# Kernel optimization log

Hardware: AMD Instinct MI355X
Metric: run time of the kernel (lower is better)

## Reference

```python
import jax, jax.numpy as jnp
import numpy as np

V, C, BLK = 32000, 512, 2048
B, T = 4, 2048
EPS = 1e-5


def _layernorm(x, g, b):
    mu = jnp.mean(x, axis=-1, keepdims=True)
    var = jnp.mean(jnp.square(x - mu), axis=-1, keepdims=True)
    return (x - mu) * jax.lax.rsqrt(var + EPS) * g + b


def setup_inputs() -> dict:
    key = jax.random.key(0)
    ks = jax.random.split(key, 16)
    s = 0.02
    return {
        "idx": jax.random.randint(ks[0], (B, T), 0, V),
        "targets": jax.random.randint(ks[1], (B, T), 0, V),
        "tok_emb": jax.random.normal(ks[2], (V, C), jnp.float32) * s,
        "pos_emb": jax.random.normal(ks[3], (BLK, C), jnp.float32) * s,
        "Wk": jax.random.normal(ks[4], (C, C), jnp.float32) * s,
        "Wq": jax.random.normal(ks[5], (C, C), jnp.float32) * s,
        "Wv": jax.random.normal(ks[6], (C, C), jnp.float32) * s,
        "W1": jax.random.normal(ks[7], (4 * C, C), jnp.float32) * s,
        "b1": jnp.zeros((4 * C,), jnp.float32),
        "W2": jax.random.normal(ks[8], (C, 4 * C), jnp.float32) * s,
        "b2": jnp.zeros((C,), jnp.float32),
        "g1": jnp.ones((C,), jnp.float32),
        "beta1": jnp.zeros((C,), jnp.float32),
        "g2": jnp.ones((C,), jnp.float32),
        "beta2": jnp.zeros((C,), jnp.float32),
        "Wlm": jax.random.normal(ks[9], (V, C), jnp.float32) * s,
        "blm": jnp.zeros((V,), jnp.float32),
    }


def reference(idx, targets, tok_emb, pos_emb, Wk, Wq, Wv, W1, b1, W2, b2,
              g1, beta1, g2, beta2, Wlm, blm):
    # embeddings
    x = tok_emb[idx] + pos_emb[:T]  # [B,T,C]
    # single-head causal self-attention (dropout = identity, eval mode)
    h = _layernorm(x, g1, beta1)
    q = jnp.einsum('btc,dc->btd', h, Wq)
    k = jnp.einsum('btc,dc->btd', h, Wk)
    v = jnp.einsum('btc,dc->btd', h, Wv)
    wei = jnp.einsum('btd,bsd->bts', q, k) * (C ** -0.5)  # [B,T,T]
    mask = jnp.tril(jnp.ones((T, T), bool))
    wei = jnp.where(mask, wei, -jnp.inf)
    wei = jax.nn.softmax(wei, axis=-1)
    x = x + jnp.einsum('bts,bsd->btd', wei, v)
    # FFN
    h2 = _layernorm(x, g2, beta2)
    ff = jax.nn.relu(jnp.einsum('btc,fc->btf', h2, W1) + b1)
    x = x + jnp.einsum('btf,cf->btc', ff, W2) + b2
    # lm head + cross-entropy
    logits = (jnp.einsum('btc,vc->btv', x, Wlm) + blm).reshape(B * T, V)
    logp = jax.nn.log_softmax(logits, axis=-1)
    loss = -jnp.mean(jnp.take_along_axis(logp, targets.reshape(-1, 1), axis=1))
    return logits, loss
```

## Files before the change

kernel.cpp:

```cpp
#include <hip/hip_runtime.h>

typedef __bf16 bf16;
typedef __bf16 bf16x8 __attribute__((ext_vector_type(8)));
typedef float  f32x4  __attribute__((ext_vector_type(4)));

#define NB 4
#define NT 2048
#define NC 512
#define NV 32000
#define NROWS (NB*NT)
#define NCHUNK (NV/128)
#define LNEPS 1e-5f

static __device__ __forceinline__ void load_lds16(const bf16* g, bf16* l) {
  __builtin_amdgcn_global_load_lds(
      (const __attribute__((address_space(1))) void*)g,
      (__attribute__((address_space(3))) void*)l, 16, 0, 0);
}

__global__ __launch_bounds__(256)
void cvt_kernel(const float* __restrict__ in, bf16* __restrict__ out, int n8) {
  long i = (long)blockIdx.x * 256 + threadIdx.x;
  long stride = (long)gridDim.x * 256;
  for (; i < n8; i += stride) {
    const float* p = in + i * 8;
    f32x4 a = *(const f32x4*)p;
    f32x4 b = *(const f32x4*)(p + 4);
    bf16x8 o;
    o[0]=(bf16)a.x; o[1]=(bf16)a.y; o[2]=(bf16)a.z; o[3]=(bf16)a.w;
    o[4]=(bf16)b.x; o[5]=(bf16)b.y; o[6]=(bf16)b.z; o[7]=(bf16)b.w;
    *(bf16x8*)(out + i*8) = o;
  }
}

__global__ __launch_bounds__(64)
void embed_kernel(const int* __restrict__ idx, const float* __restrict__ tok,
                  const float* __restrict__ pos, float* __restrict__ x0) {
  int row = blockIdx.x;
  int t = row & (NT-1);
  int id = idx[row];
  int lane = threadIdx.x;
  const float* tr = tok + (long)id*NC + lane*8;
  const float* pr = pos + (long)t*NC + lane*8;
  f32x4 a0 = *(const f32x4*)tr, a1 = *(const f32x4*)(tr+4);
  f32x4 p0 = *(const f32x4*)pr, p1 = *(const f32x4*)(pr+4);
  f32x4 r0 = a0 + p0, r1 = a1 + p1;
  float* o = x0 + (long)row*NC + lane*8;
  *(f32x4*)o = r0; *(f32x4*)(o+4) = r1;
}

__global__ __launch_bounds__(64)
void ln_kernel(const float* __restrict__ x, const float* __restrict__ gw,
               const float* __restrict__ bw, bf16* __restrict__ out) {
  int row = blockIdx.x;
  int lane = threadIdx.x;
  const float* xr = x + (long)row*NC + lane*8;
  f32x4 a = *(const f32x4*)xr;
  f32x4 b = *(const f32x4*)(xr+4);
  float v[8] = {a.x,a.y,a.z,a.w,b.x,b.y,b.z,b.w};
  float s = 0.f;
  #pragma unroll
  for (int j=0;j<8;++j) s += v[j];
  #pragma unroll
  for (int m=32;m>=1;m>>=1) s += __shfl_xor(s, m);
  float mu = s * (1.f/NC);
  float sq = 0.f;
  #pragma unroll
  for (int j=0;j<8;++j) { v[j] -= mu; sq += v[j]*v[j]; }
  #pragma unroll
  for (int m=32;m>=1;m>>=1) sq += __shfl_xor(sq, m);
  float rs = rsqrtf(sq * (1.f/NC) + LNEPS);
  const float* gp = gw + lane*8;
  const float* bp = bw + lane*8;
  f32x4 g0 = *(const f32x4*)gp, g1 = *(const f32x4*)(gp+4);
  f32x4 b0 = *(const f32x4*)bp, b1 = *(const f32x4*)(bp+4);
  float gg[8] = {g0.x,g0.y,g0.z,g0.w,g1.x,g1.y,g1.z,g1.w};
  float bb[8] = {b0.x,b0.y,b0.z,b0.w,b1.x,b1.y,b1.z,b1.w};
  bf16x8 o;
  #pragma unroll
  for (int j=0;j<8;++j) o[j] = (bf16)(v[j]*rs*gg[j] + bb[j]);
  *(bf16x8*)(out + (long)row*NC + lane*8) = o;
}

__global__ __launch_bounds__(256)
void transpose_kernel(const bf16* __restrict__ v, bf16* __restrict__ vt) {
  __shared__ bf16 tile[64][66];
  int b = blockIdx.z;
  int t0 = blockIdx.x*64, c0 = blockIdx.y*64;
  int tid = threadIdx.x;
  int r = tid >> 2, ch = (tid & 3) * 16;
  const bf16* src = v + ((long)b*NT + t0 + r)*NC + c0 + ch;
  #pragma unroll
  for (int i=0;i<16;++i) tile[r][ch+i] = src[i];
  __syncthreads();
  bf16x8 o0, o1;
  #pragma unroll
  for (int i=0;i<8;++i) o0[i] = tile[ch+i][r];
  #pragma unroll
  for (int i=0;i<8;++i) o1[i] = tile[ch+8+i][r];
  bf16* dst = vt + ((long)b*NC + c0 + r)*NT + t0 + ch;
  *(bf16x8*)dst = o0;
  *(bf16x8*)(dst+8) = o1;
}

__global__ __launch_bounds__(256)
void softmax_kernel(float* __restrict__ S) {
  const int row = blockIdx.x;
  const int t = row & (NT-1);
  const int tid = threadIdx.x;
  float* sr = S + (long)row*NT;
  bf16* pr = (bf16*)S + (long)row*(2*NT);
  const float scale = 0.044194173824159216f;
  f32x4 v0 = *(const f32x4*)(sr + tid*8);
  f32x4 v1 = *(const f32x4*)(sr + tid*8 + 4);
  float v[8] = {v0.x,v0.y,v0.z,v0.w,v1.x,v1.y,v1.z,v1.w};
  int cb = tid*8;
  float mx = -1e30f;
  #pragma unroll
  for (int j=0;j<8;++j) {
    v[j] = (cb + j <= t) ? v[j]*scale : -1e30f;
    mx = fmaxf(mx, v[j]);
  }
  __shared__ float redm[4];
  #pragma unroll
  for (int m=32;m>=1;m>>=1) mx = fmaxf(mx, __shfl_xor(mx, m));
  if ((tid & 63) == 0) redm[tid>>6] = mx;
  __syncthreads();
  mx = fmaxf(fmaxf(redm[0],redm[1]), fmaxf(redm[2],redm[3]));
  float e[8]; float s = 0.f;
  #pragma unroll
  for (int j=0;j<8;++j) { e[j] = (cb + j <= t) ? __expf(v[j]-mx) : 0.f; s += e[j]; }
  __shared__ float reds[4];
  #pragma unroll
  for (int m=32;m>=1;m>>=1) s += __shfl_xor(s, m);
  if ((tid & 63) == 0) reds[tid>>6] = s;
  __syncthreads();
  s = reds[0]+reds[1]+reds[2]+reds[3];
  float inv = 1.f/s;
  bf16x8 o;
  #pragma unroll
  for (int j=0;j<8;++j) o[j] = (bf16)(e[j]*inv);
  *(bf16x8*)(pr + cb) = o;
}

enum { EPI_F32=0, EPI_BF16=1, EPI_BIAS_RELU_BF16=2, EPI_BIAS_RES_BF16=3, EPI_RES_F32=4, EPI_LMHEAD=5 };

template<int EPI>
__global__ __launch_bounds__(256)
void gemm_bt(const bf16* __restrict__ A, const bf16* __restrict__ B, int K,
             long lda, long ldb, long sAb, long sBb,
             float* __restrict__ outf, bf16* __restrict__ outb, long ldo, long sOb,
             const float* __restrict__ bias,
             const float* __restrict__ res, long ldr, long sRb,
             float* __restrict__ pmax, float* __restrict__ psum, int nchunk) {
  __shared__ bf16 As[128*32] __attribute__((aligned(16)));
  __shared__ bf16 Bs[128*32] __attribute__((aligned(16)));
  const int tid = threadIdx.x;
  const int wave = tid >> 6;
  const int lane = tid & 63;
  const int bm = blockIdx.y, bn = blockIdx.x, bz = blockIdx.z;
  const int wr = wave >> 1, wc = wave & 1;
  const int l15 = lane & 15, g = lane >> 4;

  const bf16* Ab = A + (long)bz*sAb + (long)bm*128*lda;
  const bf16* Bb = B + (long)bz*sBb + (long)bn*128*ldb;

  f32x4 acc[4][4] = {};

  const int r0 = tid >> 2,          c0 = tid & 3;
  const int r1 = (256+tid) >> 2,    c1 = tid & 3;
  bf16* lA0 = As + (wave*64)*8;
  bf16* lB0 = Bs + (wave*64)*8;
  bf16* lA1 = As + (256 + wave*64)*8;
  bf16* lB1 = Bs + (256 + wave*64)*8;

  for (int k0 = 0; k0 < K; k0 += 32) {
    __syncthreads();
    load_lds16(Ab + (long)r0*lda + k0 + c0*8, lA0);
    load_lds16(Bb + (long)r0*ldb + k0 + c0*8, lB0);
    load_lds16(Ab + (long)r1*lda + k0 + c1*8, lA1);
    load_lds16(Bb + (long)r1*ldb + k0 + c1*8, lB1);
    __syncthreads();
    bf16x8 af[4], bfr[4];
    #pragma unroll
    for (int m=0;m<4;++m)
      af[m] = *(const bf16x8*)(As + ((wr*64 + m*16 + l15)*32 + g*8));
    #pragma unroll
    for (int n=0;n<4;++n)
      bfr[n] = *(const bf16x8*)(Bs + ((wc*64 + n*16 + l15)*32 + g*8));
    #pragma unroll
    for (int m=0;m<4;++m)
      #pragma unroll
      for (int n=0;n<4;++n)
        acc[m][n] = __builtin_amdgcn_mfma_f32_16x16x32_bf16(af[m], bfr[n], acc[m][n], 0, 0, 0);
  }

  const long rowbase = (long)bm*128 + wr*64;
  const long colbase = (long)bn*128 + wc*64;

  if constexpr (EPI == EPI_LMHEAD) {
    __shared__ float redm[2][128];
    __shared__ float reds[2][128];
    #pragma unroll
    for (int m=0;m<4;++m) {
      #pragma unroll
      for (int n=0;n<4;++n) {
        long c = colbase + n*16 + l15;
        float bv = bias[c];
        #pragma unroll
        for (int reg=0;reg<4;++reg) {
          acc[m][n][reg] += bv;
          long rr = rowbase + m*16 + g*4 + reg;
          outf[rr*ldo + c] = acc[m][n][reg];
        }
      }
    }
    #pragma unroll
    for (int m=0;m<4;++m) {
      #pragma unroll
      for (int reg=0;reg<4;++reg) {
        float mx = -1e30f;
        #pragma unroll
        for (int n=0;n<4;++n) mx = fmaxf(mx, acc[m][n][reg]);
        #pragma unroll
        for (int msk=8;msk>=1;msk>>=1) mx = fmaxf(mx, __shfl_xor(mx, msk));
        float se = 0.f;
        #pragma unroll
        for (int n=0;n<4;++n) se += __expf(acc[m][n][reg] - mx);
        #pragma unroll
        for (int msk=8;msk>=1;msk>>=1) se += __shfl_xor(se, msk);
        if (l15 == 0) {
          int lr = wr*64 + m*16 + g*4 + reg;
          redm[wc][lr] = mx;
          reds[wc][lr] = se;
        }
      }
    }
    __syncthreads();
    if (tid < 128) {
      float m0 = redm[0][tid], m1 = redm[1][tid];
      float M = fmaxf(m0, m1);
      float Sv = reds[0][tid]*__expf(m0 - M) + reds[1][tid]*__expf(m1 - M);
      long row = (long)bm*128 + tid;
      pmax[row*nchunk + bn] = M;
      psum[row*nchunk + bn] = Sv;
    }
  } else {
    #pragma unroll
    for (int m=0;m<4;++m) {
      #pragma unroll
      for (int n=0;n<4;++n) {
        long c = colbase + n*16 + l15;
        #pragma unroll
        for (int reg=0;reg<4;++reg) {
          long rr = rowbase + m*16 + g*4 + reg;
          float v = acc[m][n][reg];
          if constexpr (EPI == EPI_F32) {
            outf[(long)bz*sOb + rr*ldo + c] = v;
          } else if constexpr (EPI == EPI_BF16) {
            outb[(long)bz*sOb + rr*ldo + c] = (bf16)v;
          } else if constexpr (EPI == EPI_BIAS_RELU_BF16) {
            v += bias[c];
            v = fmaxf(v, 0.f);
            outb[rr*ldo + c] = (bf16)v;
          } else if constexpr (EPI == EPI_BIAS_RES_BF16) {
            v += bias[c] + res[rr*ldr + c];
            outb[rr*ldo + c] = (bf16)v;
          } else if constexpr (EPI == EPI_RES_F32) {
            v += res[(long)bz*sRb + rr*ldr + c];
            outf[(long)bz*sOb + rr*ldo + c] = v;
          }
        }
      }
    }
  }
}

__global__ __launch_bounds__(256)
void loss1_kernel(const float* __restrict__ pmax, const float* __restrict__ psum,
                  const float* __restrict__ logits, const int* __restrict__ targets,
                  float* __restrict__ rowloss) {
  int row = blockIdx.x;
  int tid = threadIdx.x;
  int lane = tid & 63, wv = tid >> 6;
  float cm = (tid < NCHUNK) ? pmax[(long)row*NCHUNK + tid] : -1e30f;
  float cs = (tid < NCHUNK) ? psum[(long)row*NCHUNK + tid] : 0.f;
  float mx = cm;
  #pragma unroll
  for (int m=32;m>=1;m>>=1) mx = fmaxf(mx, __shfl_xor(mx, m));
  __shared__ float rm[4];
  if (lane == 0) rm[wv] = mx;
  __syncthreads();
  float M = fmaxf(fmaxf(rm[0],rm[1]), fmaxf(rm[2],rm[3]));
  float sc = cs * __expf(cm - M);
  #pragma unroll
  for (int m=32;m>=1;m>>=1) sc += __shfl_xor(sc, m);
  __shared__ float rs_[4];
  if (lane == 0) rs_[wv] = sc;
  __syncthreads();
  if (tid == 0) {
    float Sv = rs_[0]+rs_[1]+rs_[2]+rs_[3];
    float lse = M + logf(Sv);
    int tgt = targets[row];
    float lg = logits[(long)row*NV + tgt];
    rowloss[row] = lse - lg;
  }
}

__global__ __launch_bounds__(256)
void loss2_kernel(const float* __restrict__ rowloss, float* __restrict__ out) {
  int tid = threadIdx.x;
  float s = 0.f;
  for (int i = tid; i < NROWS; i += 256) s += rowloss[i];
  #pragma unroll
  for (int m=32;m>=1;m>>=1) s += __shfl_xor(s, m);
  __shared__ float rs_[4];
  if ((tid & 63) == 0) rs_[tid>>6] = s;
  __syncthreads();
  if (tid == 0) out[0] = (rs_[0]+rs_[1]+rs_[2]+rs_[3]) * (1.f/NROWS);
}

extern "C" void kernel_launch(void* const* d_in, const int* in_sizes, int n_in,
                              void* d_out, int out_size, void* d_ws, size_t ws_size,
                              hipStream_t stream) {
  const int*   idx  = (const int*)d_in[0];
  const int*   tgt  = (const int*)d_in[1];
  const float* tok  = (const float*)d_in[2];
  const float* pos  = (const float*)d_in[3];
  const float* Wk   = (const float*)d_in[4];
  const float* Wq   = (const float*)d_in[5];
  const float* Wv   = (const float*)d_in[6];
  const float* W1   = (const float*)d_in[7];
  const float* b1   = (const float*)d_in[8];
  const float* W2   = (const float*)d_in[9];
  const float* b2   = (const float*)d_in[10];
  const float* g1   = (const float*)d_in[11];
  const float* be1  = (const float*)d_in[12];
  const float* g2   = (const float*)d_in[13];
  const float* be2  = (const float*)d_in[14];
  const float* Wlm  = (const float*)d_in[15];
  const float* blm  = (const float*)d_in[16];

  float* logits = (float*)d_out;
  float* loss   = logits + (long)NROWS*NV;

  char* w = (char*)d_ws;
  auto alloc = [&](size_t bytes) -> char* {
    char* p = w; w += (bytes + 255) & ~(size_t)255; return p;
  };
  bf16* wqb  = (bf16*)alloc((size_t)NC*NC*2);
  bf16* wkb  = (bf16*)alloc((size_t)NC*NC*2);
  bf16* wvb  = (bf16*)alloc((size_t)NC*NC*2);
  bf16* w1b  = (bf16*)alloc((size_t)4*NC*NC*2);
  bf16* w2b  = (bf16*)alloc((size_t)4*NC*NC*2);
  bf16* wlmb = (bf16*)alloc((size_t)NV*NC*2);
  float* x0  = (float*)alloc((size_t)NROWS*NC*4);
  bf16* h1b  = (bf16*)alloc((size_t)NROWS*NC*2);
  bf16* qb   = (bf16*)alloc((size_t)NROWS*NC*2);
  bf16* kb   = (bf16*)alloc((size_t)NROWS*NC*2);
  bf16* vb   = (bf16*)alloc((size_t)NROWS*NC*2);
  bf16* vtb  = (bf16*)alloc((size_t)NROWS*NC*2);
  float* Sb  = (float*)alloc((size_t)NB*NT*NT*4);
  float* x1  = (float*)alloc((size_t)NROWS*NC*4);
  bf16* h2b  = (bf16*)alloc((size_t)NROWS*NC*2);
  bf16* ffb  = (bf16*)alloc((size_t)NROWS*4*NC*2);
  bf16* x2b  = (bf16*)alloc((size_t)NROWS*NC*2);
  float* pmax = (float*)alloc((size_t)NROWS*NCHUNK*4);
  float* psum = (float*)alloc((size_t)NROWS*NCHUNK*4);
  float* rowloss = (float*)alloc((size_t)NROWS*4);

  auto cvt = [&](const float* in, bf16* out, long n) {
    int n8 = (int)(n/8);
    int blocks = (n8 + 255)/256; if (blocks > 2048) blocks = 2048;
    cvt_kernel<<<blocks, 256, 0, stream>>>(in, out, n8);
  };
  cvt(Wq, wqb, (long)NC*NC);
  cvt(Wk, wkb, (long)NC*NC);
  cvt(Wv, wvb, (long)NC*NC);
  cvt(W1, w1b, (long)4*NC*NC);
  cvt(W2, w2b, (long)4*NC*NC);
  cvt(Wlm, wlmb, (long)NV*NC);

  embed_kernel<<<NROWS, 64, 0, stream>>>(idx, tok, pos, x0);
  ln_kernel<<<NROWS, 64, 0, stream>>>(x0, g1, be1, h1b);

  gemm_bt<EPI_BF16><<<dim3(4,64,1), 256, 0, stream>>>(
      h1b, wqb, NC, NC, NC, 0, 0, nullptr, qb, NC, 0,
      nullptr, nullptr, 0, 0, nullptr, nullptr, 0);
  gemm_bt<EPI_BF16><<<dim3(4,64,1), 256, 0, stream>>>(
      h1b, wkb, NC, NC, NC, 0, 0, nullptr, kb, NC, 0,
      nullptr, nullptr, 0, 0, nullptr, nullptr, 0);
  gemm_bt<EPI_BF16><<<dim3(4,64,1), 256, 0, stream>>>(
      h1b, wvb, NC, NC, NC, 0, 0, nullptr, vb, NC, 0,
      nullptr, nullptr, 0, 0, nullptr, nullptr, 0);

  transpose_kernel<<<dim3(NT/64, NC/64, NB), 256, 0, stream>>>(vb, vtb);

  gemm_bt<EPI_F32><<<dim3(16,16,NB), 256, 0, stream>>>(
      qb, kb, NC, NC, NC, (long)NT*NC, (long)NT*NC,
      Sb, nullptr, NT, (long)NT*NT,
      nullptr, nullptr, 0, 0, nullptr, nullptr, 0);

  softmax_kernel<<<NROWS, 256, 0, stream>>>(Sb);

  gemm_bt<EPI_RES_F32><<<dim3(4,16,NB), 256, 0, stream>>>(
      (const bf16*)Sb, vtb, NT, 2*NT, NT, (long)NT*2*NT, (long)NC*NT,
      x1, nullptr, NC, (long)NT*NC,
      nullptr, x0, NC, (long)NT*NC, nullptr, nullptr, 0);

  ln_kernel<<<NROWS, 64, 0, stream>>>(x1, g2, be2, h2b);

  gemm_bt<EPI_BIAS_RELU_BF16><<<dim3(16,64,1), 256, 0, stream>>>(
      h2b, w1b, NC, NC, NC, 0, 0, nullptr, ffb, 4*NC, 0,
      b1, nullptr, 0, 0, nullptr, nullptr, 0);

  gemm_bt<EPI_BIAS_RES_BF16><<<dim3(4,64,1), 256, 0, stream>>>(
      ffb, w2b, 4*NC, 4*NC, 4*NC, 0, 0, nullptr, x2b, NC, 0,
      b2, x1, NC, 0, nullptr, nullptr, 0);

  gemm_bt<EPI_LMHEAD><<<dim3(NCHUNK,64,1), 256, 0, stream>>>(
      x2b, wlmb, NC, NC, NC, 0, 0, logits, nullptr, NV, 0,
      blm, nullptr, 0, 0, pmax, psum, NCHUNK);

  loss1_kernel<<<NROWS, 256, 0, stream>>>(pmax, psum, logits, tgt, rowloss);
  loss2_kernel<<<1, 256, 0, stream>>>(rowloss, loss);
}
```

Baseline: 887.9 us.

## Replace GEMM with 256x256 double-buffered swizzled kernel, fuse QKV, skip causal tiles

Replaces the 128x128 single-buffered GEMM with a 256x256-tile, 512-thread kernel. It uses 128KB of double-buffered LDS with XOR swizzle, interleaved barriers and setprio to overlap global->LDS loads with MFMA. The Q/K/V projections are fused into one GEMM with a concatenated weight. The causal QK^T skips upper-triangle tiles and the PV GEMM limits K to the causal extent. The LM head uses XCD-aware block remapping. Risks include lower occupancy, added register pressure from 32 accumulators per thread, and nkt_eff needing to be even for the two-tile loop.

```diff
diff --git a/kernel.cpp b/kernel.cpp
--- a/kernel.cpp
+++ b/kernel.cpp
@@ -9,13 +9,20 @@
 #define NC 512
 #define NV 32000
 #define NROWS (NB*NT)
-#define NCHUNK (NV/128)
+#define NCHUNK (NV/256)
 #define LNEPS 1e-5f
-
-static __device__ __forceinline__ void load_lds16(const bf16* g, bf16* l) {
+#define SMEM_B 131072
+
+static __device__ __forceinline__ void load_lds16(const bf16* g, char* l) {
   __builtin_amdgcn_global_load_lds(
       (const __attribute__((address_space(1))) void*)g,
       (__attribute__((address_space(3))) void*)l, 16, 0, 0);
+}
+
+static __device__ __forceinline__ void bar() {
+  asm volatile("" ::: "memory");
+  __builtin_amdgcn_s_barrier();
+  asm volatile("" ::: "memory");
 }
 
 __global__ __launch_bounds__(256)
@@ -83,13 +90,13 @@
 }
 
 __global__ __launch_bounds__(256)
-void transpose_kernel(const bf16* __restrict__ v, bf16* __restrict__ vt) {
+void transpose_kernel(const bf16* __restrict__ v, long ldv, bf16* __restrict__ vt) {
   __shared__ bf16 tile[64][66];
   int b = blockIdx.z;
   int t0 = blockIdx.x*64, c0 = blockIdx.y*64;
   int tid = threadIdx.x;
   int r = tid >> 2, ch = (tid & 3) * 16;
-  const bf16* src = v + ((long)b*NT + t0 + r)*NC + c0 + ch;
+  const bf16* src = v + ((long)b*NT + t0 + r)*ldv + c0 + ch;
   #pragma unroll
   for (int i=0;i<16;++i) tile[r][ch+i] = src[i];
   __syncthreads();
@@ -145,134 +152,274 @@
 
 enum { EPI_F32=0, EPI_BF16=1, EPI_BIAS_RELU_BF16=2, EPI_BIAS_RES_BF16=3, EPI_RES_F32=4, EPI_LMHEAD=5 };
 
-template<int EPI>
-__global__ __launch_bounds__(256)
-void gemm_bt(const bf16* __restrict__ A, const bf16* __restrict__ B, int K,
+template<int EPI, bool CAUSAL=false, bool KLIMIT=false, bool SWZ=false>
+__global__ __launch_bounds__(512,2)
+void gemm256(const bf16* __restrict__ A, const bf16* __restrict__ B, int nkt,
              long lda, long ldb, long sAb, long sBb,
              float* __restrict__ outf, bf16* __restrict__ outb, long ldo, long sOb,
              const float* __restrict__ bias,
              const float* __restrict__ res, long ldr, long sRb,
-             float* __restrict__ pmax, float* __restrict__ psum, int nchunk) {
-  __shared__ bf16 As[128*32] __attribute__((aligned(16)));
-  __shared__ bf16 Bs[128*32] __attribute__((aligned(16)));
+             float* __restrict__ pmax, float* __restrict__ psum) {
+  extern __shared__ char smem[];
+  int bn = blockIdx.x, bm = blockIdx.y;
+  const int bz = blockIdx.z;
+  if constexpr (SWZ) {
+    int gx = gridDim.x, nwg = gx * gridDim.y;
+    int flat = bm * gx + bn;
+    int q = nwg >> 3, r = nwg & 7;
+    int xcd = flat & 7, pos = flat >> 3;
+    int wgid = (xcd < r ? xcd*(q+1) : r*(q+1) + (xcd-r)*q) + pos;
+    bn = wgid % gx; bm = wgid / gx;
+  }
+  if constexpr (CAUSAL) { if (bn > bm) return; }
+  int nkt_eff = nkt;
+  if constexpr (KLIMIT) { int c = (bm+1)*4; if (c < nkt_eff) nkt_eff = c; }
+
   const int tid = threadIdx.x;
-  const int wave = tid >> 6;
-  const int lane = tid & 63;
-  const int bm = blockIdx.y, bn = blockIdx.x, bz = blockIdx.z;
-  const int wr = wave >> 1, wc = wave & 1;
+  const int wid = tid >> 6, lane = tid & 63;
+  const int wr = wid >> 2, wc = wid & 3;
   const int l15 = lane & 15, g = lane >> 4;
 
-  const bf16* Ab = A + (long)bz*sAb + (long)bm*128*lda;
-  const bf16* Bb = B + (long)bz*sBb + (long)bn*128*ldb;
-
-  f32x4 acc[4][4] = {};
-
-  const int r0 = tid >> 2,          c0 = tid & 3;
-  const int r1 = (256+tid) >> 2,    c1 = tid & 3;
-  bf16* lA0 = As + (wave*64)*8;
-  bf16* lB0 = Bs + (wave*64)*8;
-  bf16* lA1 = As + (256 + wave*64)*8;
-  bf16* lB1 = Bs + (256 + wave*64)*8;
-
-  for (int k0 = 0; k0 < K; k0 += 32) {
-    __syncthreads();
-    load_lds16(Ab + (long)r0*lda + k0 + c0*8, lA0);
-    load_lds16(Bb + (long)r0*ldb + k0 + c0*8, lB0);
-    load_lds16(Ab + (long)r1*lda + k0 + c1*8, lA1);
-    load_lds16(Bb + (long)r1*ldb + k0 + c1*8, lB1);
-    __syncthreads();
-    bf16x8 af[4], bfr[4];
-    #pragma unroll
-    for (int m=0;m<4;++m)
-      af[m] = *(const bf16x8*)(As + ((wr*64 + m*16 + l15)*32 + g*8));
-    #pragma unroll
-    for (int n=0;n<4;++n)
-      bfr[n] = *(const bf16x8*)(Bs + ((wc*64 + n*16 + l15)*32 + g*8));
-    #pragma unroll
-    for (int m=0;m<4;++m)
-      #pragma unroll
-      for (int n=0;n<4;++n)
-        acc[m][n] = __builtin_amdgcn_mfma_f32_16x16x32_bf16(af[m], bfr[n], acc[m][n], 0, 0, 0);
+  const bf16* Ab = A + (long)bz*sAb + (long)bm*256*lda;
+  const bf16* Bb = B + (long)bz*sBb + (long)bn*256*ldb;
+
+  const int colsw = ((tid & 7) * 8) ^ ((tid & 32) ? 16 : 0);
+  const bf16* A0 = Ab + (long)(tid >> 3)*lda + colsw;
+  const bf16* B0 = Bb + (long)(tid >> 3)*ldb + colsw;
+
+  auto stage = [&](int ab, int t, int h, int slot) {
+    char* dst = smem + slot*65536 + ab*32768 + h*16384 + wid*1024;
+    const bf16* s0 = (ab ? B0 : A0) + (long)(h*128)*(ab ? ldb : lda) + (long)t*64;
+    load_lds16(s0, dst);
+    load_lds16(s0 + 64*(ab ? ldb : lda), dst + 8192);
+  };
+
+  const char* sm = smem;
+  auto aLoad = [&](int slot, int m, int kk) -> bf16x8 {
+    int row = m*16 + l15;
+    int b = row*128 + kk*64 + g*16;
+    b ^= (row & 4) << 3;
+    return *(const bf16x8*)(sm + slot*65536 + wr*16384 + b);
+  };
+  auto bLoad = [&](int slot, int n, int kk) -> bf16x8 {
+    int row = (wc & 1)*64 + n*16 + l15;
+    int b = row*128 + kk*64 + g*16;
+    b ^= (row & 4) << 3;
+    return *(const bf16x8*)(sm + slot*65536 + 32768 + (wc >> 1)*16384 + b);
+  };
+
+  f32x4 acc[8][4] = {};
+
+  stage(0, 0, 0, 0);
+  stage(0, 0, 1, 0);
+  stage(1, 0, 0, 0);
+  stage(1, 0, 1, 0);
+  stage(0, 1, 0, 1);
+  asm volatile("s_waitcnt vmcnt(2)" ::: "memory");
+  bar();
+
+  const int niter = nkt_eff >> 1;
+  for (int it = 0; it < niter; ++it) {
+    const int t0 = 2*it, t1 = 2*it + 1;
+    const int tn0 = (t0+2 < nkt_eff) ? t0+2 : nkt_eff-1;
+    const int tn1 = (t1+2 < nkt_eff) ? t1+2 : nkt_eff-1;
+    bf16x8 a0[4][2], a1[4][2], b0[2][2], b1[2][2];
+
+    #pragma unroll
+    for (int m=0;m<4;++m) { a0[m][0]=aLoad(0,m,0); a0[m][1]=aLoad(0,m,1); }
+    #pragma unroll
+    for (int n=0;n<2;++n) { b0[n][0]=bLoad(0,n,0); b0[n][1]=bLoad(0,n,1); }
+    stage(0, t1, 1, 1);
+    bar();
+    __builtin_amdgcn_s_setprio(1);
+    #pragma unroll
+    for (int m=0;m<4;++m)
+      #pragma unroll
+      for (int n=0;n<2;++n) {
+        acc[m][n] = __builtin_amdgcn_mfma_f32_16x16x32_bf16(a0[m][0], b0[n][0], acc[m][n],0,0,0);
+        acc[m][n] = __builtin_amdgcn_mfma_f32_16x16x32_bf16(a0[m][1], b0[n][1], acc[m][n],0,0,0);
+      }
+    __builtin_amdgcn_s_setprio(0);
+    bar();
+
+    #pragma unroll
+    for (int n=0;n<2;++n) { b1[n][0]=bLoad(0,n+2,0); b1[n][1]=bLoad(0,n+2,1); }
+    stage(1, t1, 0, 1);
+    bar();
+    __builtin_amdgcn_s_setprio(1);
+    #pragma unroll
+    for (int m=0;m<4;++m)
+      #pragma unroll
+      for (int n=0;n<2;++n) {
+        acc[m][n+2] = __builtin_amdgcn_mfma_f32_16x16x32_bf16(a0[m][0], b1[n][0], acc[m][n+2],0,0,0);
+        acc[m][n+2] = __builtin_amdgcn_mfma_f32_16x16x32_bf16(a0[m][1], b1[n][1], acc[m][n+2],0,0,0);
+      }
+    __builtin_amdgcn_s_setprio(0);
+    bar();
+
+    #pragma unroll
+    for (int m=0;m<4;++m) { a1[m][0]=aLoad(0,m+4,0); a1[m][1]=aLoad(0,m+4,1); }
+    stage(1, t1, 1, 1);
+    bar();
+    __builtin_amdgcn_s_setprio(1);
+    #pragma unroll
+    for (int m=0;m<4;++m)
+      #pragma unroll
+      for (int n=0;n<2;++n) {
+        acc[m+4][n+2] = __builtin_amdgcn_mfma_f32_16x16x32_bf16(a1[m][0], b1[n][0], acc[m+4][n+2],0,0,0);
+        acc[m+4][n+2] = __builtin_amdgcn_mfma_f32_16x16x32_bf16(a1[m][1], b1[n][1], acc[m+4][n+2],0,0,0);
+      }
+    __builtin_amdgcn_s_setprio(0);
+    bar();
+
+    stage(0, tn0, 0, 0);
+    asm volatile("s_waitcnt vmcnt(2)" ::: "memory");
+    bar();
+    __builtin_amdgcn_s_setprio(1);
+    #pragma unroll
+    for (int m=0;m<4;++m)
+      #pragma unroll
+      for (int n=0;n<2;++n) {
+        acc[m+4][n] = __builtin_amdgcn_mfma_f32_16x16x32_bf16(a1[m][0], b0[n][0], acc[m+4][n],0,0,0);
+        acc[m+4][n] = __builtin_amdgcn_mfma_f32_16x16x32_bf16(a1[m][1], b0[n][1], acc[m+4][n],0,0,0);
+      }
+    __builtin_amdgcn_s_setprio(0);
+    bar();
+
+    #pragma unroll
+    for (int m=0;m<4;++m) { a0[m][0]=aLoad(1,m,0); a0[m][1]=aLoad(1,m,1); }
+    #pragma unroll
+    for (int n=0;n<2;++n) { b0[n][0]=bLoad(1,n,0); b0[n][1]=bLoad(1,n,1); }
+    stage(0, tn0, 1, 0);
+    bar();
+    __builtin_amdgcn_s_setprio(1);
+    #pragma unroll
+    for (int m=0;m<4;++m)
+      #pragma unroll
+      for (int n=0;n<2;++n) {
+        acc[m][n] = __builtin_amdgcn_mfma_f32_16x16x32_bf16(a0[m][0], b0[n][0], acc[m][n],0,0,0);
+        acc[m][n] = __builtin_amdgcn_mfma_f32_16x16x32_bf16(a0[m][1], b0[n][1], acc[m][n],0,0,0);
+      }
+    __builtin_amdgcn_s_setprio(0);
+    bar();
+
+    #pragma unroll
+    for (int n=0;n<2;++n) { b1[n][0]=bLoad(1,n+2,0); b1[n][1]=bLoad(1,n+2,1); }
+    stage(1, tn0, 0, 0);
+    bar();
+    __builtin_amdgcn_s_setprio(1);
+    #pragma unroll
+    for (int m=0;m<4;++m)
+      #pragma unroll
+      for (int n=0;n<2;++n) {
+        acc[m][n+2] = __builtin_amdgcn_mfma_f32_16x16x32_bf16(a0[m][0], b1[n][0], acc[m][n+2],0,0,0);
+        acc[m][n+2] = __builtin_amdgcn_mfma_f32_16x16x32_bf16(a0[m][1], b1[n][1], acc[m][n+2],0,0,0);
+      }
+    __builtin_amdgcn_s_setprio(0);
+    bar();
+
+    #pragma unroll
+    for (int m=0;m<4;++m) { a1[m][0]=aLoad(1,m+4,0); a1[m][1]=aLoad(1,m+4,1); }
+    stage(1, tn0, 1, 0);
+    bar();
+    __builtin_amdgcn_s_setprio(1);
+    #pragma unroll
+    for (int m=0;m<4;++m)
+      #pragma unroll
+      for (int n=0;n<2;++n) {
+        acc[m+4][n+2] = __builtin_amdgcn_mfma_f32_16x16x32_bf16(a1[m][0], b1[n][0], acc[m+4][n+2],0,0,0);
+        acc[m+4][n+2] = __builtin_amdgcn_mfma_f32_16x16x32_bf16(a1[m][1], b1[n][1], acc[m+4][n+2],0,0,0);
+      }
+    __builtin_amdgcn_s_setprio(0);
+    bar();
+
+    stage(0, tn1, 0, 1);
+    asm volatile("s_waitcnt vmcnt(2)" ::: "memory");
+    bar();
+    __builtin_amdgcn_s_setprio(1);
+    #pragma unroll
+    for (int m=0;m<4;++m)
+      #pragma unroll
+      for (int n=0;n<2;++n) {
+        acc[m+4][n] = __builtin_amdgcn_mfma_f32_16x16x32_bf16(a1[m][0], b0[n][0], acc[m+4][n],0,0,0);
+        acc[m+4][n] = __builtin_amdgcn_mfma_f32_16x16x32_bf16(a1[m][1], b0[n][1], acc[m+4][n],0,0,0);
+      }
+    __builtin_amdgcn_s_setprio(0);
+    bar();
   }
 
-  const long rowbase = (long)bm*128 + wr*64;
-  const long colbase = (long)bn*128 + wc*64;
+  const long rowbase = (long)bm*256 + wr*128;
+  const long colbase = (long)bn*256 + wc*64;
 
   if constexpr (EPI == EPI_LMHEAD) {
-    __shared__ float redm[2][128];
-    __shared__ float reds[2][128];
-    #pragma unroll
-    for (int m=0;m<4;++m) {
+    #pragma unroll
+    for (int m=0;m<8;++m)
       #pragma unroll
       for (int n=0;n<4;++n) {
         long c = colbase + n*16 + l15;
         float bv = bias[c];
         #pragma unroll
-        for (int reg=0;reg<4;++reg) {
-          acc[m][n][reg] += bv;
-          long rr = rowbase + m*16 + g*4 + reg;
-          outf[rr*ldo + c] = acc[m][n][reg];
+        for (int q_=0;q_<4;++q_) {
+          acc[m][n][q_] += bv;
+          long rr = rowbase + m*16 + g*4 + q_;
+          outf[rr*ldo + c] = acc[m][n][q_];
         }
       }
-    }
-    #pragma unroll
-    for (int m=0;m<4;++m) {
-      #pragma unroll
-      for (int reg=0;reg<4;++reg) {
-        float mx = -1e30f;
-        #pragma unroll
-        for (int n=0;n<4;++n) mx = fmaxf(mx, acc[m][n][reg]);
+    __syncthreads();
+    float* redm = (float*)smem;
+    float* reds = redm + 1024;
+    #pragma unroll
+    for (int m=0;m<8;++m)
+      #pragma unroll
+      for (int q_=0;q_<4;++q_) {
+        float mx = fmaxf(fmaxf(acc[m][0][q_], acc[m][1][q_]),
+                         fmaxf(acc[m][2][q_], acc[m][3][q_]));
         #pragma unroll
         for (int msk=8;msk>=1;msk>>=1) mx = fmaxf(mx, __shfl_xor(mx, msk));
         float se = 0.f;
         #pragma unroll
-        for (int n=0;n<4;++n) se += __expf(acc[m][n][reg] - mx);
+        for (int n=0;n<4;++n) se += __expf(acc[m][n][q_] - mx);
         #pragma unroll
         for (int msk=8;msk>=1;msk>>=1) se += __shfl_xor(se, msk);
         if (l15 == 0) {
-          int lr = wr*64 + m*16 + g*4 + reg;
-          redm[wc][lr] = mx;
-          reds[wc][lr] = se;
+          int rloc = wr*128 + m*16 + g*4 + q_;
+          redm[wc*256 + rloc] = mx;
+          reds[wc*256 + rloc] = se;
         }
       }
-    }
     __syncthreads();
-    if (tid < 128) {
-      float m0 = redm[0][tid], m1 = redm[1][tid];
-      float M = fmaxf(m0, m1);
-      float Sv = reds[0][tid]*__expf(m0 - M) + reds[1][tid]*__expf(m1 - M);
-      long row = (long)bm*128 + tid;
-      pmax[row*nchunk + bn] = M;
-      psum[row*nchunk + bn] = Sv;
+    if (tid < 256) {
+      float m0=redm[tid], m1=redm[256+tid], m2=redm[512+tid], m3=redm[768+tid];
+      float M = fmaxf(fmaxf(m0,m1), fmaxf(m2,m3));
+      float Sv = reds[tid]*__expf(m0-M) + reds[256+tid]*__expf(m1-M)
+               + reds[512+tid]*__expf(m2-M) + reds[768+tid]*__expf(m3-M);
+      long row = (long)bm*256 + tid;
+      pmax[row*NCHUNK + bn] = M;
+      psum[row*NCHUNK + bn] = Sv;
     }
   } else {
     #pragma unroll
-    for (int m=0;m<4;++m) {
+    for (int m=0;m<8;++m)
       #pragma unroll
       for (int n=0;n<4;++n) {
         long c = colbase + n*16 + l15;
         #pragma unroll
-        for (int reg=0;reg<4;++reg) {
-          long rr = rowbase + m*16 + g*4 + reg;
-          float v = acc[m][n][reg];
+        for (int q_=0;q_<4;++q_) {
+          long rr = rowbase + m*16 + g*4 + q_;
+          float v = acc[m][n][q_];
           if constexpr (EPI == EPI_F32) {
             outf[(long)bz*sOb + rr*ldo + c] = v;
           } else if constexpr (EPI == EPI_BF16) {
             outb[(long)bz*sOb + rr*ldo + c] = (bf16)v;
           } else if constexpr (EPI == EPI_BIAS_RELU_BF16) {
-            v += bias[c];
-            v = fmaxf(v, 0.f);
-            outb[rr*ldo + c] = (bf16)v;
+            outb[rr*ldo + c] = (bf16)fmaxf(v + bias[c], 0.f);
           } else if constexpr (EPI == EPI_BIAS_RES_BF16) {
-            v += bias[c] + res[rr*ldr + c];
-            outb[rr*ldo + c] = (bf16)v;
+            outb[rr*ldo + c] = (bf16)(v + bias[c] + res[rr*ldr + c]);
           } else if constexpr (EPI == EPI_RES_F32) {
-            v += res[(long)bz*sRb + rr*ldr + c];
-            outf[(long)bz*sOb + rr*ldo + c] = v;
+            outf[(long)bz*sOb + rr*ldo + c] = v + res[(long)bz*sRb + rr*ldr + c];
           }
         }
       }
-    }
   }
 }
 
@@ -348,35 +495,44 @@
   auto alloc = [&](size_t bytes) -> char* {
     char* p = w; w += (bytes + 255) & ~(size_t)255; return p;
   };
-  bf16* wqb  = (bf16*)alloc((size_t)NC*NC*2);
-  bf16* wkb  = (bf16*)alloc((size_t)NC*NC*2);
-  bf16* wvb  = (bf16*)alloc((size_t)NC*NC*2);
-  bf16* w1b  = (bf16*)alloc((size_t)4*NC*NC*2);
-  bf16* w2b  = (bf16*)alloc((size_t)4*NC*NC*2);
-  bf16* wlmb = (bf16*)alloc((size_t)NV*NC*2);
-  float* x0  = (float*)alloc((size_t)NROWS*NC*4);
-  bf16* h1b  = (bf16*)alloc((size_t)NROWS*NC*2);
-  bf16* qb   = (bf16*)alloc((size_t)NROWS*NC*2);
-  bf16* kb   = (bf16*)alloc((size_t)NROWS*NC*2);
-  bf16* vb   = (bf16*)alloc((size_t)NROWS*NC*2);
-  bf16* vtb  = (bf16*)alloc((size_t)NROWS*NC*2);
-  float* Sb  = (float*)alloc((size_t)NB*NT*NT*4);
-  float* x1  = (float*)alloc((size_t)NROWS*NC*4);
-  bf16* h2b  = (bf16*)alloc((size_t)NROWS*NC*2);
-  bf16* ffb  = (bf16*)alloc((size_t)NROWS*4*NC*2);
-  bf16* x2b  = (bf16*)alloc((size_t)NROWS*NC*2);
+  bf16* wqkvb = (bf16*)alloc((size_t)3*NC*NC*2);
+  bf16* w1b   = (bf16*)alloc((size_t)4*NC*NC*2);
+  bf16* w2b   = (bf16*)alloc((size_t)4*NC*NC*2);
+  bf16* wlmb  = (bf16*)alloc((size_t)NV*NC*2);
+  float* x0   = (float*)alloc((size_t)NROWS*NC*4);
+  bf16* h1b   = (bf16*)alloc((size_t)NROWS*NC*2);
+  bf16* qkvb  = (bf16*)alloc((size_t)NROWS*3*NC*2);
+  bf16* vtb   = (bf16*)alloc((size_t)NROWS*NC*2);
+  float* Sb   = (float*)alloc((size_t)NB*NT*NT*4);
+  float* x1   = (float*)alloc((size_t)NROWS*NC*4);
+  bf16* h2b   = (bf16*)alloc((size_t)NROWS*NC*2);
+  bf16* ffb   = (bf16*)alloc((size_t)NROWS*4*NC*2);
+  bf16* x2b   = (bf16*)alloc((size_t)NROWS*NC*2);
   float* pmax = (float*)alloc((size_t)NROWS*NCHUNK*4);
   float* psum = (float*)alloc((size_t)NROWS*NCHUNK*4);
   float* rowloss = (float*)alloc((size_t)NROWS*4);
+
+  hipFuncSetAttribute((const void*)gemm256<EPI_BF16,false,false,false>,
+                      hipFuncAttributeMaxDynamicSharedMemorySize, SMEM_B);
+  hipFuncSetAttribute((const void*)gemm256<EPI_F32,true,false,false>,
+                      hipFuncAttributeMaxDynamicSharedMemorySize, SMEM_B);
+  hipFuncSetAttribute((const void*)gemm256<EPI_RES_F32,false,true,false>,
+                      hipFuncAttributeMaxDynamicSharedMemorySize, SMEM_B);
+  hipFuncSetAttribute((const void*)gemm256<EPI_BIAS_RELU_BF16,false,false,false>,
+                      hipFuncAttributeMaxDynamicSharedMemorySize, SMEM_B);
+  hipFuncSetAttribute((const void*)gemm256<EPI_BIAS_RES_BF16,false,false,false>,
+                      hipFuncAttributeMaxDynamicSharedMemorySize, SMEM_B);
+  hipFuncSetAttribute((const void*)gemm256<EPI_LMHEAD,false,false,true>,
+                      hipFuncAttributeMaxDynamicSharedMemorySize, SMEM_B);
 
   auto cvt = [&](const float* in, bf16* out, long n) {
     int n8 = (int)(n/8);
     int blocks = (n8 + 255)/256; if (blocks > 2048) blocks = 2048;
     cvt_kernel<<<blocks, 256, 0, stream>>>(in, out, n8);
   };
-  cvt(Wq, wqb, (long)NC*NC);
-  cvt(Wk, wkb, (long)NC*NC);
-  cvt(Wv, wvb, (long)NC*NC);
+  cvt(Wq, wqkvb, (long)NC*NC);
+  cvt(Wk, wqkvb + (long)NC*NC, (long)NC*NC);
+  cvt(Wv, wqkvb + (long)2*NC*NC, (long)NC*NC);
   cvt(W1, w1b, (long)4*NC*NC);
   cvt(W2, w2b, (long)4*NC*NC);
   cvt(Wlm, wlmb, (long)NV*NC);
@@ -384,43 +540,37 @@
   embed_kernel<<<NROWS, 64, 0, stream>>>(idx, tok, pos, x0);
   ln_kernel<<<NROWS, 64, 0, stream>>>(x0, g1, be1, h1b);
 
-  gemm_bt<EPI_BF16><<<dim3(4,64,1), 256, 0, stream>>>(
-      h1b, wqb, NC, NC, NC, 0, 0, nullptr, qb, NC, 0,
-      nullptr, nullptr, 0, 0, nullptr, nullptr, 0);
-  gemm_bt<EPI_BF16><<<dim3(4,64,1), 256, 0, stream>>>(
-      h1b, wkb, NC, NC, NC, 0, 0, nullptr, kb, NC, 0,
-      nullptr, nullptr, 0, 0, nullptr, nullptr, 0);
-  gemm_bt<EPI_BF16><<<dim3(4,64,1), 256, 0, stream>>>(
-      h1b, wvb, NC, NC, NC, 0, 0, nullptr, vb, NC, 0,
-      nullptr, nullptr, 0, 0, nullptr, nullptr, 0);
-
-  transpose_kernel<<<dim3(NT/64, NC/64, NB), 256, 0, stream>>>(vb, vtb);
-
-  gemm_bt<EPI_F32><<<dim3(16,16,NB), 256, 0, stream>>>(
-      qb, kb, NC, NC, NC, (long)NT*NC, (long)NT*NC,
+  gemm256<EPI_BF16><<<dim3(6,32,1), 512, SMEM_B, stream>>>(
+      h1b, wqkvb, 8, NC, NC, 0, 0, nullptr, qkvb, 3*NC, 0,
+      nullptr, nullptr, 0, 0, nullptr, nullptr);
+
+  transpose_kernel<<<dim3(NT/64, NC/64, NB), 256, 0, stream>>>(qkvb + 2*NC, 3*NC, vtb);
+
+  gemm256<EPI_F32,true><<<dim3(8,8,NB), 512, SMEM_B, stream>>>(
+      qkvb, qkvb + NC, 8, 3*NC, 3*NC, (long)NT*3*NC, (long)NT*3*NC,
       Sb, nullptr, NT, (long)NT*NT,
-      nullptr, nullptr, 0, 0, nullptr, nullptr, 0);
+      nullptr, nullptr, 0, 0, nullptr, nullptr);
 
   softmax_kernel<<<NROWS, 256, 0, stream>>>(Sb);
 
-  gemm_bt<EPI_RES_F32><<<dim3(4,16,NB), 256, 0, stream>>>(
-      (const bf16*)Sb, vtb, NT, 2*NT, NT, (long)NT*2*NT, (long)NC*NT,
+  gemm256<EPI_RES_F32,false,true><<<dim3(2,8,NB), 512, SMEM_B, stream>>>(
+      (const bf16*)Sb, vtb, 32, 2*NT, NT, (long)NT*2*NT, (long)NC*NT,
       x1, nullptr, NC, (long)NT*NC,
-      nullptr, x0, NC, (long)NT*NC, nullptr, nullptr, 0);
+      nullptr, x0, NC, (long)NT*NC, nullptr, nullptr);
 
   ln_kernel<<<NROWS, 64, 0, stream>>>(x1, g2, be2, h2b);
 
-  gemm_bt<EPI_BIAS_RELU_BF16><<<dim3(16,64,1), 256, 0, stream>>>(
-      h2b, w1b, NC, NC, NC, 0, 0, nullptr, ffb, 4*NC, 0,
-      b1, nullptr, 0, 0, nullptr, nullptr, 0);
-
-  gemm_bt<EPI_BIAS_RES_BF16><<<dim3(4,64,1), 256, 0, stream>>>(
-      ffb, w2b, 4*NC, 4*NC, 4*NC, 0, 0, nullptr, x2b, NC, 0,
-      b2, x1, NC, 0, nullptr, nullptr, 0);
-
-  gemm_bt<EPI_LMHEAD><<<dim3(NCHUNK,64,1), 256, 0, stream>>>(
-      x2b, wlmb, NC, NC, NC, 0, 0, logits, nullptr, NV, 0,
-      blm, nullptr, 0, 0, pmax, psum, NCHUNK);
+  gemm256<EPI_BIAS_RELU_BF16><<<dim3(8,32,1), 512, SMEM_B, stream>>>(
+      h2b, w1b, 8, NC, NC, 0, 0, nullptr, ffb, 4*NC, 0,
+      b1, nullptr, 0, 0, nullptr, nullptr);
+
+  gemm256<EPI_BIAS_RES_BF16><<<dim3(2,32,1), 512, SMEM_B, stream>>>(
+      ffb, w2b, 32, 4*NC, 4*NC, 0, 0, nullptr, x2b, NC, 0,
+      b2, x1, NC, 0, nullptr, nullptr);
+
+  gemm256<EPI_LMHEAD,false,false,true><<<dim3(NCHUNK,32,1), 512, SMEM_B, stream>>>(
+      x2b, wlmb, 8, NC, NC, 0, 0, logits, nullptr, NV, 0,
+      blm, nullptr, 0, 0, pmax, psum);
 
   loss1_kernel<<<NROWS, 256, 0, stream>>>(pmax, psum, logits, tgt, rowloss);
   loss2_kernel<<<1, 256, 0, stream>>>(rowloss, loss);
```

Result: no change. 897.9 us (+1.1%).
